# Kernel optimization log

Hardware: AMD Instinct MI355X
Metric: run time of the kernel (lower is better)

## Reference

```python
import jax, jax.numpy as jnp
import numpy as np

B, S, D, H = 4, 2048, 1024, 16
HD = D // H  # head_dim = 64


def setup_inputs() -> dict:
    key = jax.random.key(0)
    k_x, k_m, k_wi, k_bi, k_wo, k_bo = jax.random.split(key, 6)
    x = jax.random.normal(k_x, (B, S, D), dtype=jnp.float32)
    mask = jax.random.randint(k_m, (B, S), 0, 2, dtype=jnp.int32)
    # Keras Dense: kernel shape (in, out), glorot-ish scale; bias zeros-ish (random small here)
    w_in = jax.random.normal(k_wi, (D, 3 * D), dtype=jnp.float32) * (1.0 / np.sqrt(D))
    b_in = jax.random.normal(k_bi, (3 * D,), dtype=jnp.float32) * 0.02
    w_out = jax.random.normal(k_wo, (D, D), dtype=jnp.float32) * (1.0 / np.sqrt(D))
    b_out = jax.random.normal(k_bo, (D,), dtype=jnp.float32) * 0.02
    return {"x": x, "w_in": w_in, "b_in": b_in, "w_out": w_out, "b_out": b_out, "mask": mask}


def reference(x, w_in, b_in, w_out, b_out, mask):
    b, s, _ = x.shape
    scale = jnp.asarray(HD ** (-0.5), dtype=x.dtype)
    qkv = x @ w_in + b_in                              # (B, S, 3D)
    qkv = qkv.reshape(b, s, 3, H, HD).transpose(2, 0, 3, 1, 4)  # (3, B, H, S, HD)
    q, k, v = qkv[0], qkv[1], qkv[2]
    q = q * scale
    attn = jnp.einsum("bhqd,bhkd->bhqk", q, k)         # (B, H, S, S)
    neg_inf = jnp.asarray(float("-inf"), dtype=attn.dtype)
    attn_mask = jnp.where(mask[:, None, None, :] > 0, jnp.zeros((), attn.dtype), neg_inf)
    attn = jax.nn.softmax(attn + attn_mask, axis=-1)
    out = jnp.einsum("bhqk,bhkd->bhqd", attn, v)        # (B, H, S, HD)
    out = out.transpose(0, 2, 1, 3).reshape(b, s, D)
    return out @ w_out + b_out
```

## Files before the change

kernel.cpp:

```cpp
#include <hip/hip_runtime.h>

#define B_  4
#define S_  2048
#define D_  1024
#define H_  16
#define HD_ 64
#define BH_ (B_*H_)
#define QSCALE 0.18033688f

typedef _Float16 h16;
typedef _Float16 h4 __attribute__((ext_vector_type(4)));
typedef _Float16 h8 __attribute__((ext_vector_type(8)));
typedef float    f32x4 __attribute__((ext_vector_type(4)));

#define EXP2(x) __builtin_amdgcn_exp2f(x)

__device__ __forceinline__ void gload16(const h16* g, h16* l) {
  __builtin_amdgcn_global_load_lds(
      (const __attribute__((address_space(1))) unsigned int*)g,
      (__attribute__((address_space(3))) unsigned int*)l, 16, 0, 0);
}

__global__ __launch_bounds__(256)
void prep_k(const float* __restrict__ x, const float* __restrict__ w_in,
            const float* __restrict__ b_in, const int* __restrict__ mask,
            h16* __restrict__ xc, h16* __restrict__ WinT,
            h16* __restrict__ binc, int* __restrict__ posmap,
            int* __restrict__ nvalid) {
  __shared__ __align__(16) char smem[2212];
  int blk = blockIdx.x;
  int t = threadIdx.x;
  if (blk < 4) {
    int* partial = (int*)smem;
    int b = blk;
    const int* mb = mask + b * S_;
    int base = t * 8;
    int loc[8], cnt = 0;
#pragma unroll
    for (int j = 0; j < 8; j++) { loc[j] = cnt; cnt += (mb[base + j] != 0); }
    partial[t] = cnt;
    __syncthreads();
    for (int off = 1; off < 256; off <<= 1) {
      int v = (t >= off) ? partial[t - off] : 0;
      __syncthreads();
      partial[t] += v;
      __syncthreads();
    }
    int excl = (t == 0) ? 0 : partial[t - 1];
#pragma unroll
    for (int j = 0; j < 8; j++)
      posmap[b * S_ + base + j] = (mb[base + j] != 0) ? (excl + loc[j]) : -1;
    if (t == 255) nvalid[b] = partial[255];
  } else if (blk < 6) {
    int idx = ((blk - 4) * 256 + t) * 8;
    if (idx + 8 <= 3 * D_) {
      float4 f0 = *(const float4*)(b_in + idx);
      float4 f1 = *(const float4*)(b_in + idx + 4);
      h16 tmp[8] = {(h16)f0.x, (h16)f0.y, (h16)f0.z, (h16)f0.w,
                    (h16)f1.x, (h16)f1.y, (h16)f1.z, (h16)f1.w};
      *(h8*)(binc + idx) = *(h8*)tmp;
    }
  } else if (blk < 4102) {
    int idx = ((blk - 6) * 256 + t) * 8;
    float4 f0 = *(const float4*)(x + idx);
    float4 f1 = *(const float4*)(x + idx + 4);
    h16 tmp[8] = {(h16)f0.x, (h16)f0.y, (h16)f0.z, (h16)f0.w,
                  (h16)f1.x, (h16)f1.y, (h16)f1.z, (h16)f1.w};
    *(h8*)(xc + idx) = *(h8*)tmp;
  } else {
    typedef h16 row33[33];
    row33* tile = (row33*)smem;
    int idx = blk - 4102;
    int bx = (idx % 96) * 32, by = (idx / 96) * 32;
    int tx = t & 31, ty = t >> 5;
    const int C = 3 * D_, R = D_;
#pragma unroll
    for (int i = 0; i < 32; i += 8)
      tile[ty + i][tx] = (h16)w_in[(size_t)(by + ty + i) * C + bx + tx];
    __syncthreads();
#pragma unroll
    for (int i = 0; i < 32; i += 8)
      WinT[(size_t)(bx + ty + i) * R + by + tx] = tile[tx][ty + i];
  }
}

__global__ __launch_bounds__(256)
void post_k(const float* __restrict__ w_out, const float* __restrict__ b_out,
            h16* __restrict__ WouT, h16* __restrict__ boutc) {
  __shared__ h16 tile[32][33];
  int blk = blockIdx.x;
  int t = threadIdx.x;
  if (blk < 1024) {
    int bx = (blk % 32) * 32, by = (blk / 32) * 32;
    int tx = t & 31, ty = t >> 5;
#pragma unroll
    for (int i = 0; i < 32; i += 8)
      tile[ty + i][tx] = (h16)w_out[(size_t)(by + ty + i) * D_ + bx + tx];
    __syncthreads();
#pragma unroll
    for (int i = 0; i < 32; i += 8)
      WouT[(size_t)(bx + ty + i) * D_ + by + tx] = tile[tx][ty + i];
  } else {
    int idx = t * 4;
    if (idx < D_) {
      float4 f = *(const float4*)(b_out + idx);
      h16 tmp[4] = {(h16)f.x, (h16)f.y, (h16)f.z, (h16)f.w};
      *(h4*)(boutc + idx) = *(h4*)tmp;
    }
  }
}

template <int MODE>
__global__ __launch_bounds__(256)
void gemm_bt(const h16* __restrict__ A, const h16* __restrict__ BT,
             const h16* __restrict__ bias, const int* __restrict__ posmap,
             void* __restrict__ out0v, h16* __restrict__ out1,
             h16* __restrict__ out2, int M, int N, int K) {
  const int tid  = threadIdx.x;
  const int lane = tid & 63;
  const int w    = tid >> 6;
  const int quad = lane >> 4;
  const int l16  = lane & 15;
  const int m0   = blockIdx.x * 128;
  const int n0   = blockIdx.y * 128;

  __shared__ alignas(16) h16 As[128 * 64];
  __shared__ alignas(16) h16 Bs[128 * 64];

  const f32x4 zero = {0.f, 0.f, 0.f, 0.f};
  f32x4 acc[4][4];
#pragma unroll
  for (int i = 0; i < 4; i++)
#pragma unroll
    for (int j = 0; j < 4; j++) acc[i][j] = zero;

  const int wm = (w >> 1) * 64;
  const int wn = (w & 1) * 64;
  const int sw = l16 & 7;

  for (int kt = 0; kt < K; kt += 64) {
#pragma unroll
    for (int p = 0; p < 4; p++) {
      int c   = w * 256 + p * 64 + lane;
      int row = c >> 3;
      int cc  = (c & 7) ^ (row & 7);
      gload16(&A[(size_t)(m0 + row) * K + kt + cc * 8],
              &As[(w * 256 + p * 64) * 8]);
      gload16(&BT[(size_t)(n0 + row) * K + kt + cc * 8],
              &Bs[(w * 256 + p * 64) * 8]);
    }
    __syncthreads();
#pragma unroll
    for (int kk = 0; kk < 2; kk++) {
      h8 af[4], bfr[4];
#pragma unroll
      for (int i = 0; i < 4; i++)
        af[i] = *(const h8*)(&As[(wm + i * 16 + l16) * 64 +
                                 ((kk * 4 + quad) ^ sw) * 8]);
#pragma unroll
      for (int j = 0; j < 4; j++)
        bfr[j] = *(const h8*)(&Bs[(wn + j * 16 + l16) * 64 +
                                  ((kk * 4 + quad) ^ sw) * 8]);
#pragma unroll
      for (int i = 0; i < 4; i++)
#pragma unroll
        for (int j = 0; j < 4; j++)
          acc[i][j] = __builtin_amdgcn_mfma_f32_16x16x32_f16(af[i], bfr[j],
                                                             acc[i][j], 0, 0, 0);
    }
    __syncthreads();
  }

#pragma unroll
  for (int i = 0; i < 4; i++) {
#pragma unroll
    for (int j = 0; j < 4; j++) {
      int n = n0 + wn + j * 16 + l16;
      float bv = (float)bias[n];
#pragma unroll
      for (int r = 0; r < 4; r++) {
        int m = m0 + wm + i * 16 + quad * 4 + r;
        float v = acc[i][j][r] + bv;
        if (MODE == 0) {
          h16* q0 = (h16*)out0v;
          int which = n >> 10;
          int h  = (n >> 6) & 15;
          int hd = n & 63;
          int b  = m >> 11;
          int s  = m & 2047;
          if (which == 0) {
            q0[(((size_t)(b * 16 + h)) * S_ + s) * HD_ + hd] = (h16)(v * QSCALE);
          } else {
            int pos = posmap[b * S_ + s];
            if (pos >= 0) {
              if (which == 1)
                out1[(((size_t)(b * 16 + h)) * S_ + pos) * HD_ + hd] = (h16)v;
              else
                out2[(((size_t)(b * 16 + h)) * HD_ + hd) * S_ + pos] = (h16)v;
            }
          }
        } else {
          ((float*)out0v)[(size_t)m * N + n] = v;
        }
      }
    }
  }
}

__global__ __launch_bounds__(256)
void attn_k(const h16* __restrict__ Q, const h16* __restrict__ Kc,
            const h16* __restrict__ Vtc, const int* __restrict__ nvalid,
            h16* __restrict__ out) {
  const int tid  = threadIdx.x;
  const int lane = tid & 63;
  const int w    = tid >> 6;
  const int quad = lane >> 4;
  const int l16  = lane & 15;
  const int bh   = blockIdx.y;
  const int b    = bh >> 4, h = bh & 15;
  const int q0   = blockIdx.x * 64 + w * 16;
  const int nv   = nvalid[b];
  const int sw   = l16 & 7;

  const h16* Qh = Q   + (size_t)bh * S_ * HD_;
  const h16* Kh = Kc  + (size_t)bh * S_ * HD_;
  const h16* Vh = Vtc + (size_t)bh * HD_ * S_;

  __shared__ alignas(16) h16 Ks[64 * 64];
  __shared__ alignas(16) h16 Vs[64 * 64];
  __shared__ alignas(16) h16 Pb[4][16 * 72];

  h8 bq[2];
#pragma unroll
  for (int ks = 0; ks < 2; ks++)
    bq[ks] = *(const h8*)(&Qh[(size_t)(q0 + l16) * 64 + ks * 32 + quad * 8]);

  const f32x4 zero = {0.f, 0.f, 0.f, 0.f};
  f32x4 oacc[4];
#pragma unroll
  for (int j = 0; j < 4; j++) oacc[j] = zero;
  float mst = -1e30f, lst = 0.f;

  for (int kb = 0; kb < nv; kb += 64) {
    __syncthreads();
#pragma unroll
    for (int p = 0; p < 2; p++) {
      int c   = w * 128 + p * 64 + lane;
      int row = c >> 3;
      int cc  = (c & 7) ^ (row & 7);
      gload16(&Kh[(size_t)(kb + row) * 64 + cc * 8],
              &Ks[(w * 128 + p * 64) * 8]);
      gload16(&Vh[(size_t)row * S_ + kb + cc * 8],
              &Vs[(w * 128 + p * 64) * 8]);
    }
    __syncthreads();

    f32x4 st[4];
#pragma unroll
    for (int kh = 0; kh < 4; kh++) {
      h8 ak0 = *(const h8*)(&Ks[(kh * 16 + l16) * 64 + (quad ^ sw) * 8]);
      h8 ak1 = *(const h8*)(&Ks[(kh * 16 + l16) * 64 + ((quad + 4) ^ sw) * 8]);
      f32x4 s = zero;
      s = __builtin_amdgcn_mfma_f32_16x16x32_f16(ak0, bq[0], s, 0, 0, 0);
      s = __builtin_amdgcn_mfma_f32_16x16x32_f16(ak1, bq[1], s, 0, 0, 0);
      st[kh] = s;
    }
    if (kb + 64 > nv) {
#pragma unroll
      for (int kh = 0; kh < 4; kh++)
#pragma unroll
        for (int r = 0; r < 4; r++)
          if (kb + kh * 16 + quad * 4 + r >= nv) st[kh][r] = -1e30f;
    }

    float mx = -1e30f;
#pragma unroll
    for (int kh = 0; kh < 4; kh++)
#pragma unroll
      for (int r = 0; r < 4; r++) mx = fmaxf(mx, st[kh][r]);
    mx = fmaxf(mx, __shfl_xor(mx, 16, 64));
    mx = fmaxf(mx, __shfl_xor(mx, 32, 64));
    float mnew = fmaxf(mst, mx);
    float alpha = EXP2(mst - mnew);
    float p[4][4], rs = 0.f;
#pragma unroll
    for (int kh = 0; kh < 4; kh++)
#pragma unroll
      for (int r = 0; r < 4; r++) {
        p[kh][r] = EXP2(st[kh][r] - mnew);
        rs += p[kh][r];
      }
    rs += __shfl_xor(rs, 16, 64);
    rs += __shfl_xor(rs, 32, 64);
    lst = lst * alpha + rs;
    mst = mnew;

    float al[4];
#pragma unroll
    for (int r = 0; r < 4; r++) al[r] = __shfl(alpha, quad * 4 + r, 64);
#pragma unroll
    for (int j = 0; j < 4; j++)
#pragma unroll
      for (int r = 0; r < 4; r++) oacc[j][r] *= al[r];

    h16* pb = Pb[w];
#pragma unroll
    for (int kh = 0; kh < 4; kh++) {
      h4 pk = {(h16)p[kh][0], (h16)p[kh][1], (h16)p[kh][2], (h16)p[kh][3]};
      *(h4*)(&pb[l16 * 72 + kh * 16 + quad * 4]) = pk;
    }
    h8 pa0 = *(const h8*)(&pb[l16 * 72 + quad * 8]);
    h8 pa1 = *(const h8*)(&pb[l16 * 72 + 32 + quad * 8]);

#pragma unroll
    for (int j = 0; j < 4; j++) {
      h8 bv0 = *(const h8*)(&Vs[(j * 16 + l16) * 64 + (quad ^ sw) * 8]);
      h8 bv1 = *(const h8*)(&Vs[(j * 16 + l16) * 64 + ((quad + 4) ^ sw) * 8]);
      oacc[j] = __builtin_amdgcn_mfma_f32_16x16x32_f16(pa0, bv0, oacc[j], 0, 0, 0);
      oacc[j] = __builtin_amdgcn_mfma_f32_16x16x32_f16(pa1, bv1, oacc[j], 0, 0, 0);
    }
  }

  float ls[4];
#pragma unroll
  for (int r = 0; r < 4; r++) ls[r] = __shfl(lst, quad * 4 + r, 64);
#pragma unroll
  for (int j = 0; j < 4; j++)
#pragma unroll
    for (int r = 0; r < 4; r++) {
      int row = q0 + quad * 4 + r;
      float v = oacc[j][r] / ls[r];
      out[((size_t)(b * S_ + row)) * D_ + h * 64 + j * 16 + l16] = (h16)v;
    }
}

extern "C" void kernel_launch(void* const* d_in, const int* in_sizes, int n_in,
                              void* d_out, int out_size, void* d_ws,
                              size_t ws_size, hipStream_t stream) {
  const float* x     = (const float*)d_in[0];
  const float* w_in  = (const float*)d_in[1];
  const float* b_in  = (const float*)d_in[2];
  const float* w_out = (const float*)d_in[3];
  const float* b_out = (const float*)d_in[4];
  const int*   mask  = (const int*)d_in[5];

  const size_t NT = (size_t)BH_ * S_ * HD_;
  h16* ws    = (h16*)d_ws;
  h16* Qb    = ws;
  h16* Kcb   = ws + NT;
  h16* Vtcb  = ws + 2 * NT;
  h16* xc    = ws + 3 * NT;
  h16* AOb   = ws + 3 * NT;
  h16* WouT  = Qb;
  h16* boutc = Vtcb;
  h16* WinT  = (h16*)d_out;
  h16* binc  = (h16*)d_out + 3400704;
  int* posmap = (int*)((char*)d_out + 24u * 1024 * 1024);
  int* nvalid = posmap + B_ * S_;

  prep_k<<<7174, 256, 0, stream>>>(x, w_in, b_in, mask, xc, WinT, binc,
                                   posmap, nvalid);

  gemm_bt<0><<<dim3((B_ * S_) / 128, (3 * D_) / 128), 256, 0, stream>>>(
      xc, WinT, binc, posmap, Qb, Kcb, Vtcb, B_ * S_, 3 * D_, D_);

  attn_k<<<dim3(S_ / 64, BH_), 256, 0, stream>>>(Qb, Kcb, Vtcb, nvalid, AOb);

  post_k<<<1025, 256, 0, stream>>>(w_out, b_out, WouT, boutc);

  gemm_bt<1><<<dim3((B_ * S_) / 128, D_ / 128), 256, 0, stream>>>(
      AOb, WouT, boutc, nullptr, d_out, nullptr, nullptr, B_ * S_, D_, D_);
}
```

Measured before the change: 293.4 us.

## Replace GEMM with 256x128 triple-buffered pipelined kernel using 8 waves

The QKV and output projection GEMMs now use 256x128 tiles with 512 threads and a three-stage LDS ring buffer. Loads for tile t+2 are interleaved with the MFMA quarters of tile t, gated by vmcnt waits and barriers, and s_setprio raises priority around the MFMA groups. The goal is to hide global-to-LDS latency and raise per-block compute density. In exchange the kernel uses about 144KB of LDS, which allows one block per CU, adds many barriers per K-step, and halves the grid size.

```diff
diff --git a/kernel.cpp b/kernel.cpp
--- a/kernel.cpp
+++ b/kernel.cpp
@@ -14,6 +14,7 @@
 typedef float    f32x4 __attribute__((ext_vector_type(4)));
 
 #define EXP2(x) __builtin_amdgcn_exp2f(x)
+#define BAR()   __builtin_amdgcn_s_barrier()
 
 __device__ __forceinline__ void gload16(const h16* g, h16* l) {
   __builtin_amdgcn_global_load_lds(
@@ -110,22 +111,54 @@
   }
 }
 
+__device__ __forceinline__ void stage_rounds(const h16* __restrict__ G, h16* L,
+                                             int rbase, int K, int kt,
+                                             int w, int lane, int p0, int np,
+                                             int wchunks) {
+#pragma unroll
+  for (int p = p0; p < p0 + np; ++p) {
+    int c = w * wchunks + p * 64 + lane;
+    int row = c >> 3;
+    int cc = (c & 7) ^ (row & 7);
+    gload16(&G[(size_t)(rbase + row) * K + kt + cc * 8],
+            &L[(w * wchunks + p * 64) * 8]);
+  }
+}
+
+template <int IO, int JO>
+__device__ __forceinline__ void mfma8(f32x4 (&acc)[4][4], const h8 (&afr)[2][2],
+                                      const h8 (&bfr)[4][2]) {
+  __builtin_amdgcn_s_setprio(1);
+#pragma unroll
+  for (int i = 0; i < 2; ++i)
+#pragma unroll
+    for (int j = 0; j < 2; ++j)
+#pragma unroll
+      for (int k = 0; k < 2; ++k)
+        acc[IO + i][JO + j] = __builtin_amdgcn_mfma_f32_16x16x32_f16(
+            afr[i][k], bfr[JO + j][k], acc[IO + i][JO + j], 0, 0, 0);
+  __builtin_amdgcn_s_setprio(0);
+}
+
 template <int MODE>
-__global__ __launch_bounds__(256)
-void gemm_bt(const h16* __restrict__ A, const h16* __restrict__ BT,
-             const h16* __restrict__ bias, const int* __restrict__ posmap,
-             void* __restrict__ out0v, h16* __restrict__ out1,
-             h16* __restrict__ out2, int M, int N, int K) {
+__global__ __launch_bounds__(512)
+void gemm256_k(const h16* __restrict__ A, const h16* __restrict__ BT,
+               const h16* __restrict__ bias, const int* __restrict__ posmap,
+               void* __restrict__ out0v, h16* __restrict__ out1,
+               h16* __restrict__ out2, int M, int N, int K) {
   const int tid  = threadIdx.x;
   const int lane = tid & 63;
   const int w    = tid >> 6;
   const int quad = lane >> 4;
   const int l16  = lane & 15;
-  const int m0   = blockIdx.x * 128;
+  const int m0   = blockIdx.x * 256;
   const int n0   = blockIdx.y * 128;
-
-  __shared__ alignas(16) h16 As[128 * 64];
-  __shared__ alignas(16) h16 Bs[128 * 64];
+  const int wm   = (w >> 1) * 64;
+  const int wn   = (w & 1) * 64;
+  const int sw   = l16 & 7;
+
+  __shared__ alignas(16) h16 As[3][256 * 64];
+  __shared__ alignas(16) h16 Bs[3][128 * 64];
 
   const f32x4 zero = {0.f, 0.f, 0.f, 0.f};
   f32x4 acc[4][4];
@@ -134,41 +167,69 @@
 #pragma unroll
     for (int j = 0; j < 4; j++) acc[i][j] = zero;
 
-  const int wm = (w >> 1) * 64;
-  const int wn = (w & 1) * 64;
-  const int sw = l16 & 7;
-
-  for (int kt = 0; kt < K; kt += 64) {
-#pragma unroll
-    for (int p = 0; p < 4; p++) {
-      int c   = w * 256 + p * 64 + lane;
-      int row = c >> 3;
-      int cc  = (c & 7) ^ (row & 7);
-      gload16(&A[(size_t)(m0 + row) * K + kt + cc * 8],
-              &As[(w * 256 + p * 64) * 8]);
-      gload16(&BT[(size_t)(n0 + row) * K + kt + cc * 8],
-              &Bs[(w * 256 + p * 64) * 8]);
-    }
-    __syncthreads();
-#pragma unroll
-    for (int kk = 0; kk < 2; kk++) {
-      h8 af[4], bfr[4];
-#pragma unroll
-      for (int i = 0; i < 4; i++)
-        af[i] = *(const h8*)(&As[(wm + i * 16 + l16) * 64 +
-                                 ((kk * 4 + quad) ^ sw) * 8]);
-#pragma unroll
-      for (int j = 0; j < 4; j++)
-        bfr[j] = *(const h8*)(&Bs[(wn + j * 16 + l16) * 64 +
-                                  ((kk * 4 + quad) ^ sw) * 8]);
-#pragma unroll
-      for (int i = 0; i < 4; i++)
-#pragma unroll
-        for (int j = 0; j < 4; j++)
-          acc[i][j] = __builtin_amdgcn_mfma_f32_16x16x32_f16(af[i], bfr[j],
-                                                             acc[i][j], 0, 0, 0);
-    }
-    __syncthreads();
+  const int nt = K >> 6;
+
+#pragma unroll
+  for (int tt = 0; tt < 2; ++tt) {
+    stage_rounds(A,  As[tt], m0, K, tt * 64, w, lane, 0, 4, 256);
+    stage_rounds(BT, Bs[tt], n0, K, tt * 64, w, lane, 0, 2, 128);
+  }
+
+  h8 afr[2][2];
+  h8 bfr[4][2];
+
+  for (int t = 0; t < nt; ++t) {
+    const int cb = t % 3;
+    int sb = cb + 2; if (sb >= 3) sb -= 3;
+    const h16* Ab = As[cb];
+    const h16* Bb = Bs[cb];
+    const int ktn = (t + 2) * 64;
+    const bool st = (t + 2) < nt;
+
+    if (t + 1 < nt) asm volatile("s_waitcnt vmcnt(6)" ::: "memory");
+    else            asm volatile("s_waitcnt vmcnt(0)" ::: "memory");
+    BAR();
+
+#pragma unroll
+    for (int i = 0; i < 2; ++i)
+#pragma unroll
+      for (int k = 0; k < 2; ++k)
+        afr[i][k] = *(const h8*)(Ab + (wm + i * 16 + l16) * 64 +
+                                 ((k * 4 + quad) ^ sw) * 8);
+#pragma unroll
+    for (int j = 0; j < 2; ++j)
+#pragma unroll
+      for (int k = 0; k < 2; ++k)
+        bfr[j][k] = *(const h8*)(Bb + (wn + j * 16 + l16) * 64 +
+                                 ((k * 4 + quad) ^ sw) * 8);
+    if (st) stage_rounds(A, As[sb], m0, K, ktn, w, lane, 0, 2, 256);
+    BAR();
+    mfma8<0, 0>(acc, afr, bfr);
+    BAR();
+
+#pragma unroll
+    for (int j = 2; j < 4; ++j)
+#pragma unroll
+      for (int k = 0; k < 2; ++k)
+        bfr[j][k] = *(const h8*)(Bb + (wn + j * 16 + l16) * 64 +
+                                 ((k * 4 + quad) ^ sw) * 8);
+    if (st) stage_rounds(A, As[sb], m0, K, ktn, w, lane, 2, 2, 256);
+    BAR();
+    mfma8<0, 2>(acc, afr, bfr);
+    BAR();
+
+#pragma unroll
+    for (int i = 0; i < 2; ++i)
+#pragma unroll
+      for (int k = 0; k < 2; ++k)
+        afr[i][k] = *(const h8*)(Ab + (wm + (2 + i) * 16 + l16) * 64 +
+                                 ((k * 4 + quad) ^ sw) * 8);
+    if (st) stage_rounds(BT, Bs[sb], n0, K, ktn, w, lane, 0, 2, 128);
+    BAR();
+    mfma8<2, 0>(acc, afr, bfr);
+    BAR();
+
+    mfma8<2, 2>(acc, afr, bfr);
   }
 
 #pragma unroll
@@ -361,13 +422,13 @@
   prep_k<<<7174, 256, 0, stream>>>(x, w_in, b_in, mask, xc, WinT, binc,
                                    posmap, nvalid);
 
-  gemm_bt<0><<<dim3((B_ * S_) / 128, (3 * D_) / 128), 256, 0, stream>>>(
+  gemm256_k<0><<<dim3((B_ * S_) / 256, (3 * D_) / 128), 512, 0, stream>>>(
       xc, WinT, binc, posmap, Qb, Kcb, Vtcb, B_ * S_, 3 * D_, D_);
 
   attn_k<<<dim3(S_ / 64, BH_), 256, 0, stream>>>(Qb, Kcb, Vtcb, nvalid, AOb);
 
   post_k<<<1025, 256, 0, stream>>>(w_out, b_out, WouT, boutc);
 
-  gemm_bt<1><<<dim3((B_ * S_) / 128, D_ / 128), 256, 0, stream>>>(
+  gemm256_k<1><<<dim3((B_ * S_) / 256, D_ / 128), 512, 0, stream>>>(
       AOb, WouT, boutc, nullptr, d_out, nullptr, nullptr, B_ * S_, D_, D_);
 }
```

Measured after the change: 306.0 us. 4.3% more time.

## Use 256x256-tile double-buffered GEMM with XCD-aware block mapping for QKV projection

Applied to the files above, without the earlier changes.

Replaces the 128x128 QKV projection GEMM with a 512-thread kernel that computes 256x256 output tiles. Tiles are staged with global_load_lds into XOR-swizzled LDS, double-buffered two K-steps ahead, and blocks are remapped so neighbouring tiles land on the same XCD. The aim is to cut global traffic per FLOP, hide load latency and reduce LDS bank conflicts. The cost is 128 KB of LDS per block and 128 accumulator registers per thread, which limits occupancy. The output projection GEMM is split off into its own non-templated kernel with unchanged behaviour.

```diff
diff --git a/kernel.cpp b/kernel.cpp
--- a/kernel.cpp
+++ b/kernel.cpp
@@ -110,12 +110,152 @@
   }
 }
 
-template <int MODE>
+__device__ __forceinline__ void stage_unit(const h16* __restrict__ G, h16* L,
+                                           int growbase, int K, int kcol,
+                                           int w, int lane) {
+#pragma unroll
+  for (int p2 = 0; p2 < 2; ++p2) {
+    int c = w * 128 + p2 * 64 + lane;
+    int row = c >> 3;
+    int cc = (c & 7) ^ (row & 7);
+    gload16(&G[(size_t)(growbase + row) * K + kcol + cc * 8],
+            &L[(w * 128 + p2 * 64) * 8]);
+  }
+}
+
+__global__ __launch_bounds__(512, 2)
+void gemm256_k(const h16* __restrict__ A, const h16* __restrict__ BT,
+               const h16* __restrict__ bias, const int* __restrict__ posmap,
+               h16* __restrict__ outQ, h16* __restrict__ out1,
+               h16* __restrict__ out2, int M, int N, int K) {
+  const int tid  = threadIdx.x;
+  const int lane = tid & 63;
+  const int w    = tid >> 6;
+  const int quad = lane >> 4;
+  const int l16  = lane & 15;
+  const int sw   = l16 & 7;
+
+  const int NBY = gridDim.y;
+  const int lin = blockIdx.y * gridDim.x + blockIdx.x;
+  const int xcd = lin & 7;
+  const int i_c = lin >> 3;
+  const int bx  = xcd * (gridDim.x >> 3) + i_c / NBY;
+  const int by  = i_c % NBY;
+  const int m0  = bx * 256;
+  const int n0  = by * 256;
+
+  const int wm = (w >> 2) * 128;
+  const int wn = (w & 3) * 64;
+  const int ah = (w >> 2);
+  const int bh = (w & 3) >> 1;
+  const int brow0 = ((w & 3) & 1) * 64;
+
+  __shared__ alignas(16) h16 Us[8][128 * 64];
+
+  const f32x4 zero = {0.f, 0.f, 0.f, 0.f};
+  f32x4 acc[8][4];
+#pragma unroll
+  for (int i = 0; i < 8; i++)
+#pragma unroll
+    for (int j = 0; j < 4; j++) acc[i][j] = zero;
+
+  const int nt = K >> 6;
+
+#pragma unroll
+  for (int tt = 0; tt < 2; ++tt) {
+#pragma unroll
+    for (int uid = 0; uid < 4; ++uid) {
+      h16* L = Us[tt * 4 + uid];
+      if (uid < 2) stage_unit(A,  L, m0 + uid * 128,       K, tt * 64, w, lane);
+      else         stage_unit(BT, L, n0 + (uid - 2) * 128, K, tt * 64, w, lane);
+    }
+  }
+  asm volatile("s_waitcnt vmcnt(0)" ::: "memory");
+  __syncthreads();
+
+  h8 bfr[4][2];
+  h8 afr[2][2];
+
+  for (int t = 0; t < nt; ++t) {
+    const int par = (t & 1) * 4;
+    const h16* Au = Us[par + ah];
+    const h16* Bu = Us[par + 2 + bh];
+
+#pragma unroll
+    for (int j = 0; j < 4; ++j)
+#pragma unroll
+      for (int k = 0; k < 2; ++k)
+        bfr[j][k] = *(const h8*)(Bu + (brow0 + j * 16 + l16) * 64 +
+                                 ((k * 4 + quad) ^ sw) * 8);
+
+#pragma unroll
+    for (int p = 0; p < 4; ++p) {
+#pragma unroll
+      for (int i = 0; i < 2; ++i)
+#pragma unroll
+        for (int k = 0; k < 2; ++k)
+          afr[i][k] = *(const h8*)(Au + ((2 * p + i) * 16 + l16) * 64 +
+                                   ((k * 4 + quad) ^ sw) * 8);
+      __builtin_amdgcn_s_setprio(1);
+#pragma unroll
+      for (int i = 0; i < 2; ++i)
+#pragma unroll
+        for (int j = 0; j < 4; ++j)
+#pragma unroll
+          for (int k = 0; k < 2; ++k)
+            acc[2 * p + i][j] = __builtin_amdgcn_mfma_f32_16x16x32_f16(
+                afr[i][k], bfr[j][k], acc[2 * p + i][j], 0, 0, 0);
+      __builtin_amdgcn_s_setprio(0);
+    }
+
+    asm volatile("s_waitcnt vmcnt(0)" ::: "memory");
+    __syncthreads();
+
+    if (t + 2 < nt) {
+#pragma unroll
+      for (int uid = 0; uid < 4; ++uid) {
+        h16* L = Us[par + uid];
+        if (uid < 2) stage_unit(A,  L, m0 + uid * 128,       K, (t + 2) * 64, w, lane);
+        else         stage_unit(BT, L, n0 + (uid - 2) * 128, K, (t + 2) * 64, w, lane);
+      }
+    }
+  }
+
+#pragma unroll
+  for (int i = 0; i < 8; i++) {
+#pragma unroll
+    for (int j = 0; j < 4; j++) {
+      int n = n0 + wn + j * 16 + l16;
+      float bv = (float)bias[n];
+#pragma unroll
+      for (int r = 0; r < 4; r++) {
+        int m = m0 + wm + i * 16 + quad * 4 + r;
+        float v = acc[i][j][r] + bv;
+        int which = n >> 10;
+        int h  = (n >> 6) & 15;
+        int hd = n & 63;
+        int b  = m >> 11;
+        int s  = m & 2047;
+        if (which == 0) {
+          outQ[(((size_t)(b * 16 + h)) * S_ + s) * HD_ + hd] = (h16)(v * QSCALE);
+        } else {
+          int pos = posmap[b * S_ + s];
+          if (pos >= 0) {
+            if (which == 1)
+              out1[(((size_t)(b * 16 + h)) * S_ + pos) * HD_ + hd] = (h16)v;
+            else
+              out2[(((size_t)(b * 16 + h)) * HD_ + hd) * S_ + pos] = (h16)v;
+          }
+        }
+      }
+    }
+  }
+}
+
 __global__ __launch_bounds__(256)
-void gemm_bt(const h16* __restrict__ A, const h16* __restrict__ BT,
-             const h16* __restrict__ bias, const int* __restrict__ posmap,
-             void* __restrict__ out0v, h16* __restrict__ out1,
-             h16* __restrict__ out2, int M, int N, int K) {
+void gemm_bt1(const h16* __restrict__ A, const h16* __restrict__ BT,
+              const h16* __restrict__ bias, float* __restrict__ out,
+              int M, int N, int K) {
   const int tid  = threadIdx.x;
   const int lane = tid & 63;
   const int w    = tid >> 6;
@@ -180,28 +320,7 @@
 #pragma unroll
       for (int r = 0; r < 4; r++) {
         int m = m0 + wm + i * 16 + quad * 4 + r;
-        float v = acc[i][j][r] + bv;
-        if (MODE == 0) {
-          h16* q0 = (h16*)out0v;
-          int which = n >> 10;
-          int h  = (n >> 6) & 15;
-          int hd = n & 63;
-          int b  = m >> 11;
-          int s  = m & 2047;
-          if (which == 0) {
-            q0[(((size_t)(b * 16 + h)) * S_ + s) * HD_ + hd] = (h16)(v * QSCALE);
-          } else {
-            int pos = posmap[b * S_ + s];
-            if (pos >= 0) {
-              if (which == 1)
-                out1[(((size_t)(b * 16 + h)) * S_ + pos) * HD_ + hd] = (h16)v;
-              else
-                out2[(((size_t)(b * 16 + h)) * HD_ + hd) * S_ + pos] = (h16)v;
-            }
-          }
-        } else {
-          ((float*)out0v)[(size_t)m * N + n] = v;
-        }
+        out[(size_t)m * N + n] = acc[i][j][r] + bv;
       }
     }
   }
@@ -361,13 +480,13 @@
   prep_k<<<7174, 256, 0, stream>>>(x, w_in, b_in, mask, xc, WinT, binc,
                                    posmap, nvalid);
 
-  gemm_bt<0><<<dim3((B_ * S_) / 128, (3 * D_) / 128), 256, 0, stream>>>(
+  gemm256_k<<<dim3((B_ * S_) / 256, (3 * D_) / 256), 512, 0, stream>>>(
       xc, WinT, binc, posmap, Qb, Kcb, Vtcb, B_ * S_, 3 * D_, D_);
 
   attn_k<<<dim3(S_ / 64, BH_), 256, 0, stream>>>(Qb, Kcb, Vtcb, nvalid, AOb);
 
   post_k<<<1025, 256, 0, stream>>>(w_out, b_out, WouT, boutc);
 
-  gemm_bt<1><<<dim3((B_ * S_) / 128, D_ / 128), 256, 0, stream>>>(
-      AOb, WouT, boutc, nullptr, d_out, nullptr, nullptr, B_ * S_, D_, D_);
-}
+  gemm_bt1<<<dim3((B_ * S_) / 128, D_ / 128), 256, 0, stream>>>(
+      AOb, WouT, boutc, (float*)d_out, B_ * S_, D_, D_);
+}
```

After: 312.1 us. +6.4%, slower.

## Compute K/V projection only for unmasked tokens via gathered rows

Applied to the files above, without the earlier changes.

Splits the fused QKV projection into a Q GEMM over all tokens and a K/V GEMM that gathers only valid (unmasked) token rows through a new inverse position map built in the prep kernel. Blocks past the per-batch valid count exit early, avoiding projection work for keys and values that attention never reads. It adds one kernel launch, plus gather-based loads that may coalesce less well.

```diff
diff --git a/kernel.cpp b/kernel.cpp
--- a/kernel.cpp
+++ b/kernel.cpp
@@ -26,7 +26,7 @@
             const float* __restrict__ b_in, const int* __restrict__ mask,
             h16* __restrict__ xc, h16* __restrict__ WinT,
             h16* __restrict__ binc, int* __restrict__ posmap,
-            int* __restrict__ nvalid) {
+            int* __restrict__ nvalid, int* __restrict__ invmap) {
   __shared__ __align__(16) char smem[2212];
   int blk = blockIdx.x;
   int t = threadIdx.x;
@@ -48,8 +48,15 @@
     }
     int excl = (t == 0) ? 0 : partial[t - 1];
 #pragma unroll
-    for (int j = 0; j < 8; j++)
-      posmap[b * S_ + base + j] = (mb[base + j] != 0) ? (excl + loc[j]) : -1;
+    for (int j = 0; j < 8; j++) {
+      if (mb[base + j] != 0) {
+        int pos = excl + loc[j];
+        posmap[b * S_ + base + j] = pos;
+        invmap[b * S_ + pos] = base + j;
+      } else {
+        posmap[b * S_ + base + j] = -1;
+      }
+    }
     if (t == 255) nvalid[b] = partial[255];
   } else if (blk < 6) {
     int idx = ((blk - 4) * 256 + t) * 8;
@@ -110,12 +117,10 @@
   }
 }
 
-template <int MODE>
 __global__ __launch_bounds__(256)
-void gemm_bt(const h16* __restrict__ A, const h16* __restrict__ BT,
-             const h16* __restrict__ bias, const int* __restrict__ posmap,
-             void* __restrict__ out0v, h16* __restrict__ out1,
-             h16* __restrict__ out2, int M, int N, int K) {
+void gemm_q(const h16* __restrict__ A, const h16* __restrict__ BT,
+            const h16* __restrict__ bias, h16* __restrict__ outQ) {
+  const int K = D_;
   const int tid  = threadIdx.x;
   const int lane = tid & 63;
   const int w    = tid >> 6;
@@ -177,31 +182,188 @@
     for (int j = 0; j < 4; j++) {
       int n = n0 + wn + j * 16 + l16;
       float bv = (float)bias[n];
+      int h  = (n >> 6) & 15;
+      int hd = n & 63;
 #pragma unroll
       for (int r = 0; r < 4; r++) {
         int m = m0 + wm + i * 16 + quad * 4 + r;
+        int b = m >> 11;
+        int s = m & 2047;
         float v = acc[i][j][r] + bv;
-        if (MODE == 0) {
-          h16* q0 = (h16*)out0v;
-          int which = n >> 10;
-          int h  = (n >> 6) & 15;
-          int hd = n & 63;
-          int b  = m >> 11;
-          int s  = m & 2047;
-          if (which == 0) {
-            q0[(((size_t)(b * 16 + h)) * S_ + s) * HD_ + hd] = (h16)(v * QSCALE);
-          } else {
-            int pos = posmap[b * S_ + s];
-            if (pos >= 0) {
-              if (which == 1)
-                out1[(((size_t)(b * 16 + h)) * S_ + pos) * HD_ + hd] = (h16)v;
-              else
-                out2[(((size_t)(b * 16 + h)) * HD_ + hd) * S_ + pos] = (h16)v;
-            }
-          }
-        } else {
-          ((float*)out0v)[(size_t)m * N + n] = v;
+        outQ[(((size_t)(b * 16 + h)) * S_ + s) * HD_ + hd] = (h16)(v * QSCALE);
+      }
+    }
+  }
+}
+
+__global__ __launch_bounds__(256)
+void gemm_kv(const h16* __restrict__ xc, const h16* __restrict__ BT,
+             const h16* __restrict__ bias, const int* __restrict__ invmap,
+             const int* __restrict__ nvalid,
+             h16* __restrict__ Kc, h16* __restrict__ Vtc) {
+  const int bb = blockIdx.z;
+  const int nv = nvalid[bb];
+  const int m0 = blockIdx.x * 128;
+  if (m0 >= nv) return;
+  const int K = D_;
+  const int n0 = blockIdx.y * 128;
+  const int tid  = threadIdx.x;
+  const int lane = tid & 63;
+  const int w    = tid >> 6;
+  const int quad = lane >> 4;
+  const int l16  = lane & 15;
+  const int wm = (w >> 1) * 64;
+  const int wn = (w & 1) * 64;
+  const int sw = l16 & 7;
+
+  const h16* Ab = xc + (size_t)bb * S_ * D_;
+  const int* im = invmap + bb * S_;
+
+  int srow[4];
+#pragma unroll
+  for (int p = 0; p < 4; p++) {
+    int c   = w * 256 + p * 64 + lane;
+    int row = c >> 3;
+    int m   = m0 + row;
+    srow[p] = im[m < nv ? m : nv - 1];
+  }
+
+  __shared__ alignas(16) h16 As[128 * 64];
+  __shared__ alignas(16) h16 Bs[128 * 64];
+
+  const f32x4 zero = {0.f, 0.f, 0.f, 0.f};
+  f32x4 acc[4][4];
+#pragma unroll
+  for (int i = 0; i < 4; i++)
+#pragma unroll
+    for (int j = 0; j < 4; j++) acc[i][j] = zero;
+
+  for (int kt = 0; kt < K; kt += 64) {
+#pragma unroll
+    for (int p = 0; p < 4; p++) {
+      int c   = w * 256 + p * 64 + lane;
+      int row = c >> 3;
+      int cc  = (c & 7) ^ (row & 7);
+      gload16(&Ab[(size_t)srow[p] * K + kt + cc * 8],
+              &As[(w * 256 + p * 64) * 8]);
+      gload16(&BT[(size_t)(n0 + row) * K + kt + cc * 8],
+              &Bs[(w * 256 + p * 64) * 8]);
+    }
+    __syncthreads();
+#pragma unroll
+    for (int kk = 0; kk < 2; kk++) {
+      h8 af[4], bfr[4];
+#pragma unroll
+      for (int i = 0; i < 4; i++)
+        af[i] = *(const h8*)(&As[(wm + i * 16 + l16) * 64 +
+                                 ((kk * 4 + quad) ^ sw) * 8]);
+#pragma unroll
+      for (int j = 0; j < 4; j++)
+        bfr[j] = *(const h8*)(&Bs[(wn + j * 16 + l16) * 64 +
+                                  ((kk * 4 + quad) ^ sw) * 8]);
+#pragma unroll
+      for (int i = 0; i < 4; i++)
+#pragma unroll
+        for (int j = 0; j < 4; j++)
+          acc[i][j] = __builtin_amdgcn_mfma_f32_16x16x32_f16(af[i], bfr[j],
+                                                             acc[i][j], 0, 0, 0);
+    }
+    __syncthreads();
+  }
+
+#pragma unroll
+  for (int i = 0; i < 4; i++) {
+#pragma unroll
+    for (int j = 0; j < 4; j++) {
+      int n = n0 + wn + j * 16 + l16;
+      float bv = (float)bias[n];
+      int which = n >> 10;
+      int h  = (n >> 6) & 15;
+      int hd = n & 63;
+#pragma unroll
+      for (int r = 0; r < 4; r++) {
+        int m = m0 + wm + i * 16 + quad * 4 + r;
+        if (m < nv) {
+          float v = acc[i][j][r] + bv;
+          if (which == 0)
+            Kc[(((size_t)(bb * 16 + h)) * S_ + m) * HD_ + hd] = (h16)v;
+          else
+            Vtc[(((size_t)(bb * 16 + h)) * HD_ + hd) * S_ + m] = (h16)v;
         }
+      }
+    }
+  }
+}
+
+__global__ __launch_bounds__(256)
+void gemm_bt1(const h16* __restrict__ A, const h16* __restrict__ BT,
+              const h16* __restrict__ bias, float* __restrict__ out,
+              int M, int N, int K) {
+  const int tid  = threadIdx.x;
+  const int lane = tid & 63;
+  const int w    = tid >> 6;
+  const int quad = lane >> 4;
+  const int l16  = lane & 15;
+  const int m0   = blockIdx.x * 128;
+  const int n0   = blockIdx.y * 128;
+
+  __shared__ alignas(16) h16 As[128 * 64];
+  __shared__ alignas(16) h16 Bs[128 * 64];
+
+  const f32x4 zero = {0.f, 0.f, 0.f, 0.f};
+  f32x4 acc[4][4];
+#pragma unroll
+  for (int i = 0; i < 4; i++)
+#pragma unroll
+    for (int j = 0; j < 4; j++) acc[i][j] = zero;
+
+  const int wm = (w >> 1) * 64;
+  const int wn = (w & 1) * 64;
+  const int sw = l16 & 7;
+
+  for (int kt = 0; kt < K; kt += 64) {
+#pragma unroll
+    for (int p = 0; p < 4; p++) {
+      int c   = w * 256 + p * 64 + lane;
+      int row = c >> 3;
+      int cc  = (c & 7) ^ (row & 7);
+      gload16(&A[(size_t)(m0 + row) * K + kt + cc * 8],
+              &As[(w * 256 + p * 64) * 8]);
+      gload16(&BT[(size_t)(n0 + row) * K + kt + cc * 8],
+              &Bs[(w * 256 + p * 64) * 8]);
+    }
+    __syncthreads();
+#pragma unroll
+    for (int kk = 0; kk < 2; kk++) {
+      h8 af[4], bfr[4];
+#pragma unroll
+      for (int i = 0; i < 4; i++)
+        af[i] = *(const h8*)(&As[(wm + i * 16 + l16) * 64 +
+                                 ((kk * 4 + quad) ^ sw) * 8]);
+#pragma unroll
+      for (int j = 0; j < 4; j++)
+        bfr[j] = *(const h8*)(&Bs[(wn + j * 16 + l16) * 64 +
+                                  ((kk * 4 + quad) ^ sw) * 8]);
+#pragma unroll
+      for (int i = 0; i < 4; i++)
+#pragma unroll
+        for (int j = 0; j < 4; j++)
+          acc[i][j] = __builtin_amdgcn_mfma_f32_16x16x32_f16(af[i], bfr[j],
+                                                             acc[i][j], 0, 0, 0);
+    }
+    __syncthreads();
+  }
+
+#pragma unroll
+  for (int i = 0; i < 4; i++) {
+#pragma unroll
+    for (int j = 0; j < 4; j++) {
+      int n = n0 + wn + j * 16 + l16;
+      float bv = (float)bias[n];
+#pragma unroll
+      for (int r = 0; r < 4; r++) {
+        int m = m0 + wm + i * 16 + quad * 4 + r;
+        out[(size_t)m * N + n] = acc[i][j][r] + bv;
       }
     }
   }
@@ -357,17 +519,21 @@
   h16* binc  = (h16*)d_out + 3400704;
   int* posmap = (int*)((char*)d_out + 24u * 1024 * 1024);
   int* nvalid = posmap + B_ * S_;
+  int* invmap = (int*)((char*)d_out + 25u * 1024 * 1024);
 
   prep_k<<<7174, 256, 0, stream>>>(x, w_in, b_in, mask, xc, WinT, binc,
-                                   posmap, nvalid);
-
-  gemm_bt<0><<<dim3((B_ * S_) / 128, (3 * D_) / 128), 256, 0, stream>>>(
-      xc, WinT, binc, posmap, Qb, Kcb, Vtcb, B_ * S_, 3 * D_, D_);
+                                   posmap, nvalid, invmap);
+
+  gemm_q<<<dim3((B_ * S_) / 128, D_ / 128), 256, 0, stream>>>(
+      xc, WinT, binc, Qb);
+
+  gemm_kv<<<dim3(S_ / 128, (2 * D_) / 128, B_), 256, 0, stream>>>(
+      xc, WinT + (size_t)D_ * D_, binc + D_, invmap, nvalid, Kcb, Vtcb);
 
   attn_k<<<dim3(S_ / 64, BH_), 256, 0, stream>>>(Qb, Kcb, Vtcb, nvalid, AOb);
 
   post_k<<<1025, 256, 0, stream>>>(w_out, b_out, WouT, boutc);
 
-  gemm_bt<1><<<dim3((B_ * S_) / 128, D_ / 128), 256, 0, stream>>>(
-      AOb, WouT, boutc, nullptr, d_out, nullptr, nullptr, B_ * S_, D_, D_);
-}
+  gemm_bt1<<<dim3((B_ * S_) / 128, D_ / 128), 256, 0, stream>>>(
+      AOb, WouT, boutc, (float*)d_out, B_ * S_, D_, D_);
+}
```

Measured after the change: 284.9 us. -2.9%, faster.
